# Kernel tuning notes

Hardware: AMD Instinct MI355X
Metric: run time of the kernel (lower is better)

The kernel has to match this reference:

```python
import jax, jax.numpy as jnp
import numpy as np

SUB_NO = 64
SYN_BASIS_NO = 3
T_HIST = 200
T_DATA = 100000


def setup_inputs() -> dict:
    key = jax.random.key(0)
    ks = jax.random.split(key, 5)
    # strictly-lower-triangular adjacency: each subunit integrates from ancestors
    C_den = jnp.tril((jax.random.uniform(ks[0], (SUB_NO, SUB_NO)) < 0.15).astype(jnp.float32), k=-1)
    S_conv = jax.random.normal(ks[1], (T_DATA, SUB_NO), dtype=jnp.float32)
    Y_ancest = 0.1 * jax.random.normal(ks[2], (T_DATA, SUB_NO), dtype=jnp.float32)
    # sparse binary spike trains
    Z_ancest = (jax.random.uniform(ks[3], (T_DATA, SUB_NO)) < 0.05).astype(jnp.float32)
    V_o = jnp.full((1,), -69.0, dtype=jnp.float32)
    W_sub = jnp.full((SUB_NO,), 0.25, dtype=jnp.float32)
    theta_syn = jnp.zeros((SUB_NO,), dtype=jnp.float32)
    K_spike = jnp.full((SUB_NO, SYN_BASIS_NO), 0.01, dtype=jnp.float32)
    tau_spike = jnp.arange(1.6, 1.6 + SYN_BASIS_NO, dtype=jnp.float32)
    delta_spike = jnp.zeros((SUB_NO,), dtype=jnp.float32)
    return {"S_conv": S_conv, "Y_ancest": Y_ancest, "Z_ancest": Z_ancest,
            "C_den": C_den, "V_o": V_o, "W_sub": W_sub, "theta_syn": theta_syn,
            "K_spike": K_spike, "tau_spike": tau_spike, "delta_spike": delta_spike,
            "T_hist": T_HIST}


def _ancest_kernel(K_spike, tau_spike, delta_spike, T_hist):
    # t[s, k] = max(k - delta_s, 0); kern[s, k] = sum_b (t/tau_b) exp(-t/tau_b) K[s,b]
    t = jnp.arange(T_hist, dtype=jnp.float32)[None, :] - delta_spike[:, None]
    t = jnp.maximum(t, 0.0)                                  # [sub, T_hist]
    tau = jnp.exp(tau_spike)                                 # [basis]
    t_tau = t[:, None, :] / tau[None, :, None]               # [sub, basis, T_hist]
    kern = jnp.sum(t_tau * jnp.exp(-t_tau) * K_spike[:, :, None], axis=1)
    return kern                                              # [sub, T_hist]


def reference(S_conv, Y_ancest, Z_ancest, C_den, V_o, W_sub, theta_syn,
              K_spike, tau_spike, delta_spike, T_hist):
    T_data, sub_no = S_conv.shape
    kern = _ancest_kernel(K_spike, tau_spike, delta_spike, T_hist)
    kern_f = jnp.flip(kern, axis=1)                          # matches torch.flip

    # spike_ancest[t, s, k] = sum_j C_den[s,j] Z_pad[t+k, j]  ->  precontract once
    Zc = Z_ancest @ C_den.T                                  # [T, sub]
    Zc_pad = jnp.concatenate([jnp.zeros((T_hist, sub_no), Zc.dtype), Zc], axis=0)
    # depthwise VALID conv over time: filtered[t, s] = sum_k kern_f[s,k] Zc_pad[t+k, s]
    out = jax.lax.conv_general_dilated(
        Zc_pad.T[None],                                      # [1, sub, T+T_hist]
        kern_f[:, None, :],                                  # [sub, 1, T_hist]
        window_strides=(1,), padding='VALID',
        feature_group_count=sub_no,
        dimension_numbers=('NCH', 'OIH', 'NCH'))
    filtered = out[0, :, :T_data].T                          # [T, sub]

    raw = Y_ancest @ C_den.T                                 # [T, sub]
    X_in = S_conv + theta_syn + filtered + raw
    final_Y = jax.nn.sigmoid(X_in) * W_sub + V_o
    return final_Y
```

## Files before the change

### kernel.cpp

```cpp
#include <hip/hip_runtime.h>

#define SUBS  64
#define GUARD 256
#define LB    32
#define JT    8
#define LSTR  136

typedef _Float16 f16x8 __attribute__((ext_vector_type(8)));
typedef float    f32x4 __attribute__((ext_vector_type(4)));

__device__ inline f16x8 ld_frag(const float* p) {
    float4 a = *(const float4*)p;
    float4 b = *(const float4*)(p + 4);
    f16x8 f;
    f[0]=(_Float16)a.x; f[1]=(_Float16)a.y; f[2]=(_Float16)a.z; f[3]=(_Float16)a.w;
    f[4]=(_Float16)b.x; f[5]=(_Float16)b.y; f[6]=(_Float16)b.z; f[7]=(_Float16)b.w;
    return f;
}
__device__ inline uint pkh2(float a, float b) {
    union { _Float16 h[2]; uint u; } p;
    p.h[0] = (_Float16)a; p.h[1] = (_Float16)b; return p.u;
}

#define STEP3(u)                                                                 \
    _Pragma("unroll")                                                            \
    for (int b = 0; b < 3; ++b) {                                                \
        const float yn = fmaf(twr[b], y1[b], fmaf(mr2[b], y2[b], cr[b] * (u)));  \
        y2[b] = y1[b]; y1[b] = yn;                                               \
    }
#define PAIRW(wrd) {                                                             \
    union { uint u; _Float16 h[2]; } w_; w_.u = (wrd);                           \
    STEP3((float)w_.h[0]);                                                       \
    STEP3((float)w_.h[1]); }

__global__ __launch_bounds__(256, 4) void k_mm(
    const float* __restrict__ Z, const float* __restrict__ Y,
    const float* __restrict__ C,
    const float* __restrict__ K_spike, const float* __restrict__ tau_spike,
    _Float16* __restrict__ Zt, _Float16* __restrict__ Yt,
    float* __restrict__ fb, int T, int rgz, int NB)
{
    __shared__ _Float16 ztl[SUBS * LSTR];
    __shared__ _Float16 ytl[SUBS * LSTR];
    const int tid  = threadIdx.x;
    const int lane = tid & 63;
    const int wv   = tid >> 6;
    const int lr   = lane & 15;
    const int lg   = lane >> 4;
    const int t0b  = blockIdx.x * 128;

    if (blockIdx.x < 8) {
        const int tile = blockIdx.x * 4 + (tid >> 6);
        uint4 z4 = {0, 0, 0, 0};
        ((uint4*)Zt)[(size_t)tile * 64 + (tid & 63)] = z4;
        ((uint4*)Yt)[(size_t)tile * 64 + (tid & 63)] = z4;
    } else if (blockIdx.x < 18) {
        const int tile = rgz + (blockIdx.x - 8) * 4 + (tid >> 6);
        uint4 z4 = {0, 0, 0, 0};
        ((uint4*)Zt)[(size_t)tile * 64 + (tid & 63)] = z4;
        ((uint4*)Yt)[(size_t)tile * 64 + (tid & 63)] = z4;
    }
    if (blockIdx.x == 0) {
        for (int idx = tid; idx < JT * 384; idx += 256) fb[idx] = 0.f;
    }

    f16x8 bfr[4][2];
    #pragma unroll
    for (int nt = 0; nt < 4; ++nt)
        #pragma unroll
        for (int ks = 0; ks < 2; ++ks)
            bfr[nt][ks] = ld_frag(&C[(lr + 16 * nt) * 64 + ks * 32 + lg * 8]);

    #pragma unroll
    for (int g = 0; g < 2; ++g) {
        const int t0 = t0b + wv * 32 + g * 16;
        const int rowA = t0 + lr;
        const bool okA = rowA < T;
        f16x8 az[2], ay[2];
        #pragma unroll
        for (int ks = 0; ks < 2; ++ks) {
            if (okA) {
                az[ks] = ld_frag(&Z[(size_t)rowA * 64 + ks * 32 + lg * 8]);
                ay[ks] = ld_frag(&Y[(size_t)rowA * 64 + ks * 32 + lg * 8]);
            } else {
                az[ks] = (f16x8)(_Float16)0.f;
                ay[ks] = (f16x8)(_Float16)0.f;
            }
        }

        f32x4 accZ[4], accY[4];
        #pragma unroll
        for (int nt = 0; nt < 4; ++nt) { accZ[nt] = (f32x4){0,0,0,0}; accY[nt] = (f32x4){0,0,0,0}; }
        #pragma unroll
        for (int nt = 0; nt < 4; ++nt) {
            #pragma unroll
            for (int ks = 0; ks < 2; ++ks) {
                accZ[nt] = __builtin_amdgcn_mfma_f32_16x16x32_f16(az[ks], bfr[nt][ks], accZ[nt], 0, 0, 0);
                accY[nt] = __builtin_amdgcn_mfma_f32_16x16x32_f16(ay[ks], bfr[nt][ks], accY[nt], 0, 0, 0);
            }
        }

        #pragma unroll
        for (int nt = 0; nt < 4; ++nt) {
            const int sc = lr + 16 * nt;
            const int lt = wv * 32 + g * 16 + lg * 4;
            uint2 pz, py;
            pz.x = pkh2(accZ[nt][0], accZ[nt][1]);
            pz.y = pkh2(accZ[nt][2], accZ[nt][3]);
            py.x = pkh2(accY[nt][0], accY[nt][1]);
            py.y = pkh2(accY[nt][2], accY[nt][3]);
            *(uint2*)&ztl[sc * LSTR + lt] = pz;
            *(uint2*)&ytl[sc * LSTR + lt] = py;
        }
    }

    __syncthreads();

    const int gbase = (GUARD >> 3) + blockIdx.x * 16;
    #pragma unroll
    for (int it = 0; it < 4; ++it) {
        const int chunk = it * 256 + tid;
        const int row = chunk & 63;
        const int col = chunk >> 6;
        const int tb  = t0b + col * 8;
        if (tb + 7 < T) {
            ((uint4*)Zt)[(size_t)(gbase + col) * 64 + row] =
                *(const uint4*)&ztl[row * LSTR + col * 8];
            ((uint4*)Yt)[(size_t)(gbase + col) * 64 + row] =
                *(const uint4*)&ytl[row * LSTR + col * 8];
        } else {
            #pragma unroll
            for (int h = 0; h < 8; ++h)
                if (tb + h < T) {
                    Zt[(size_t)(gbase + col) * 512 + row * 8 + h] = ztl[row * LSTR + col * 8 + h];
                    Yt[(size_t)(gbase + col) * 512 + row * 8 + h] = ytl[row * LSTR + col * 8 + h];
                }
        }
    }

    const int grun = blockIdx.x * 4 + wv;
    if (grun < NB) {
        float twr[3], mr2[3], cr[3];
        #pragma unroll
        for (int b = 0; b < 3; ++b) {
            const float tau = __expf(tau_spike[b]);
            const float r   = __expf(-1.0f / tau);
            twr[b] = 2.0f * r;
            mr2[b] = -r * r;
            cr[b]  = K_spike[lane * 3 + b] / tau * r;
        }
        const uint* zr = (const uint*)ztl + lane * (LSTR / 2) + wv * 16;
        float y1[3] = {0.f, 0.f, 0.f}, y2[3] = {0.f, 0.f, 0.f};
        uint xa[8];
        #pragma unroll
        for (int k = 0; k < 8; ++k) xa[k] = zr[k];
        #pragma unroll
        for (int k = 0; k < 8; ++k) PAIRW(xa[k]);
        #pragma unroll
        for (int k = 0; k < 8; ++k) xa[k] = zr[8 + k];
        #pragma unroll
        for (int k = 0; k < 8; ++k) PAIRW(xa[k]);
        float* fout = fb + (size_t)(grun + JT) * 384;
        #pragma unroll
        for (int b = 0; b < 3; ++b) {
            fout[(2 * b)     * 64 + lane] = y1[b];
            fout[(2 * b + 1) * 64 + lane] = y2[b];
        }
    }
}

#define EMIT(o, f) {                                                             \
    const int t_ = t0 + (o);                                                     \
    if (t_ < T) {                                                                \
        union { uint u; _Float16 h[2]; } wy_; wy_.u = ywd[(o) >> 1];             \
        union { uint u; _Float16 h[2]; } wp_; wp_.u = spk[(o) >> 1];             \
        const float xin_ = (float)wy_.h[(o) & 1] + (float)wp_.h[(o) & 1] + (f);  \
        const float sig_ = 1.0f / (1.0f + __expf(-xin_));                        \
        out[(size_t)t_ * 64 + s] = fmaf(sig_, wsub, vo);                         \
    } }

__global__ __launch_bounds__(256, 3) void k_iir2(
    const _Float16* __restrict__ Zt, const _Float16* __restrict__ Yt,
    const float* __restrict__ S,
    const float* __restrict__ K_spike, const float* __restrict__ tau_spike,
    const float* __restrict__ delta_spike, const float* __restrict__ theta,
    const float* __restrict__ W, const float* __restrict__ Vo,
    const float* __restrict__ fb, float* __restrict__ out, int T, int NB)
{
    const int tid = threadIdx.x;
    const int s   = tid & 63;
    const int wv  = tid >> 6;
    const int i   = blockIdx.x * 4 + wv;
    if (i >= NB) return;
    const int t0 = i * LB;

    float twr[3], mr2[3], cr[3], taus[3];
    #pragma unroll
    for (int b = 0; b < 3; ++b) {
        const float tau = __expf(tau_spike[b]);
        taus[b] = tau;
        const float r = __expf(-1.0f / tau);
        twr[b] = 2.0f * r;
        mr2[b] = -r * r;
        cr[b]  = K_spike[s * 3 + b] / tau * r;
    }
    int dl = (int)rintf(delta_spike[s]);
    dl = min(max(dl, 0), 30);
    const float th   = theta[s];
    const float wsub = W[s];
    const float vo   = Vo[0];

    float y1[3], y2[3];

    if (__all(dl == 0)) {
        float aL[3], bL[3], cL[3], dL[3];
        #pragma unroll
        for (int b = 0; b < 3; ++b) {
            const float r   = 0.5f * twr[b];
            const float rm1 = __expf(-(float)(LB - 1) / taus[b]);
            const float rl  = rm1 * r;
            const float rp  = rl * r;
            aL[b] = (float)(LB + 1) * rl;
            bL[b] = -(float)LB * rp;
            cL[b] = (float)LB * rm1;
            dL[b] = -(float)(LB - 1) * rl;
        }
        {
            const float* fq = fb + (size_t)i * 384;
            #pragma unroll
            for (int b = 0; b < 3; ++b) {
                y1[b] = fq[(2 * b) * 64 + s];
                y2[b] = fq[(2 * b + 1) * 64 + s];
            }
        }
        #pragma unroll
        for (int j = 7; j >= 1; --j) {
            const float* fq = fb + (size_t)(i + JT - j) * 384;
            #pragma unroll
            for (int b = 0; b < 3; ++b) {
                const float f1 = fq[(2 * b) * 64 + s];
                const float f2 = fq[(2 * b + 1) * 64 + s];
                const float n1 = fmaf(aL[b], y1[b], fmaf(bL[b], y2[b], f1));
                const float n2 = fmaf(cL[b], y1[b], fmaf(dL[b], y2[b], f2));
                y1[b] = n1; y2[b] = n2;
            }
        }

        const uint4* xb = (const uint4*)Zt + (size_t)(32 + 4 * i) * 64 + s;
        const uint4 x0 = xb[0], x1 = xb[64], x2 = xb[128], x3 = xb[192];
        const uint4* yb = (const uint4*)Yt + (size_t)(32 + 4 * i) * 64 + s;
        const uint4 yv0 = yb[0], yv1 = yb[64], yv2 = yb[128], yv3 = yb[192];

        uint spk[16];
        #pragma unroll
        for (int p = 0; p < 16; ++p) {
            const int t1 = min(t0 + 2 * p,     T - 1);
            const int t2 = min(t0 + 2 * p + 1, T - 1);
            spk[p] = pkh2(S[(size_t)t1 * 64 + s] + th, S[(size_t)t2 * 64 + s] + th);
        }

        const uint xw[15] = { x0.x, x0.y, x0.z, x0.w, x1.x, x1.y, x1.z, x1.w,
                              x2.x, x2.y, x2.z, x2.w, x3.x, x3.y, x3.z };
        const uint ywd[16] = { yv0.x, yv0.y, yv0.z, yv0.w, yv1.x, yv1.y, yv1.z, yv1.w,
                               yv2.x, yv2.y, yv2.z, yv2.w, yv3.x, yv3.y, yv3.z, yv3.w };

        EMIT(0, y2[0] + y2[1] + y2[2]);
        EMIT(1, y1[0] + y1[1] + y1[2]);
        #pragma unroll
        for (int w = 0; w < 15; ++w) {
            union { uint u; _Float16 h[2]; } wx; wx.u = xw[w];
            STEP3((float)wx.h[0]);
            EMIT(2 + 2 * w, y1[0] + y1[1] + y1[2]);
            STEP3((float)wx.h[1]);
            EMIT(3 + 2 * w, y1[0] + y1[1] + y1[2]);
        }
    } else {
        y1[0] = y1[1] = y1[2] = 0.f;
        y2[0] = y2[1] = y2[2] = 0.f;
        const int xi0 = t0 - 226 - dl;
        for (int k = 0; k < 224 + LB; ++k) {
            const int h = GUARD + xi0 + k;
            const float u = (float)Zt[(size_t)(h >> 3) * 512 + s * 8 + (h & 7)];
            STEP3(u);
            const int o = k - 224;
            if (o >= 0) {
                const int t = t0 + o;
                if (t < T) {
                    const int hy = GUARD + t;
                    const float yc = (float)Yt[(size_t)(hy >> 3) * 512 + s * 8 + (hy & 7)];
                    const float xin = yc + S[(size_t)t * 64 + s] + th
                                      + y1[0] + y1[1] + y1[2];
                    const float sig = 1.0f / (1.0f + __expf(-xin));
                    out[(size_t)t * 64 + s] = fmaf(sig, wsub, vo);
                }
            }
        }
    }
}

extern "C" void kernel_launch(void* const* d_in, const int* in_sizes, int n_in,
                              void* d_out, int out_size, void* d_ws, size_t ws_size,
                              hipStream_t stream)
{
    const float* S     = (const float*)d_in[0];
    const float* Y     = (const float*)d_in[1];
    const float* Z     = (const float*)d_in[2];
    const float* C     = (const float*)d_in[3];
    const float* Vo    = (const float*)d_in[4];
    const float* W     = (const float*)d_in[5];
    const float* theta = (const float*)d_in[6];
    const float* K     = (const float*)d_in[7];
    const float* tau   = (const float*)d_in[8];
    const float* delta = (const float*)d_in[9];
    const int T  = in_sizes[0] / SUBS;
    const int NB = (T + LB - 1) / LB;

    const int rgz    = (GUARD + T + 7) >> 3;
    const int ntiles = rgz + 44;
    _Float16* Zt = (_Float16*)d_ws;
    _Float16* Yt = (_Float16*)((char*)d_ws + (size_t)ntiles * 1024);
    float*    fb = (float*)((char*)d_ws + (size_t)ntiles * 2048);

    k_mm<<<(T + 127) / 128, 256, 0, stream>>>(Z, Y, C, K, tau, Zt, Yt, fb, T, rgz, NB);
    k_iir2<<<(NB + 3) / 4, 256, 0, stream>>>(Zt, Yt, S, K, tau, delta, theta,
                                             W, Vo, fb, (float*)d_out, T, NB);
}
```

Baseline: 46.55 us.

## Fold S_conv and theta into matmul stage output, vectorize partial-state layout

The first kernel now adds S_conv and theta to the Y@C^T accumulator, so it stores a single fp16 bias tile instead of Y-projection data alone. The recurrence/emit kernel then reads one combined tile and no longer loads S. The per-block IIR partial states are stored interleaved per subunit, so each is written and read with float4/float2 accesses. Guard-tile zeroing is skipped when all delays are zero, and the tail store is vectorised. This cuts global traffic in the second kernel and raises its occupancy hint, but the S loads in the first kernel are strided, and rounding S+theta to fp16 adds precision error.

```diff
diff --git a/kernel.cpp b/kernel.cpp
--- a/kernel.cpp
+++ b/kernel.cpp
@@ -35,9 +35,11 @@
 
 __global__ __launch_bounds__(256, 4) void k_mm(
     const float* __restrict__ Z, const float* __restrict__ Y,
-    const float* __restrict__ C,
+    const float* __restrict__ S, const float* __restrict__ C,
+    const float* __restrict__ theta,
     const float* __restrict__ K_spike, const float* __restrict__ tau_spike,
-    _Float16* __restrict__ Zt, _Float16* __restrict__ Yt,
+    const float* __restrict__ delta_spike,
+    _Float16* __restrict__ Zt, _Float16* __restrict__ Bt,
     float* __restrict__ fb, int T, int rgz, int NB)
 {
     __shared__ _Float16 ztl[SUBS * LSTR];
@@ -49,19 +51,25 @@
     const int lg   = lane >> 4;
     const int t0b  = blockIdx.x * 128;
 
-    if (blockIdx.x < 8) {
-        const int tile = blockIdx.x * 4 + (tid >> 6);
-        uint4 z4 = {0, 0, 0, 0};
-        ((uint4*)Zt)[(size_t)tile * 64 + (tid & 63)] = z4;
-        ((uint4*)Yt)[(size_t)tile * 64 + (tid & 63)] = z4;
-    } else if (blockIdx.x < 18) {
-        const int tile = rgz + (blockIdx.x - 8) * 4 + (tid >> 6);
-        uint4 z4 = {0, 0, 0, 0};
-        ((uint4*)Zt)[(size_t)tile * 64 + (tid & 63)] = z4;
-        ((uint4*)Yt)[(size_t)tile * 64 + (tid & 63)] = z4;
-    }
+    int dl = (int)rintf(delta_spike[lane]);
+    dl = min(max(dl, 0), 30);
+    const bool alldl0 = __all(dl == 0);
+
     if (blockIdx.x == 0) {
-        for (int idx = tid; idx < JT * 384; idx += 256) fb[idx] = 0.f;
+        for (int idx = tid; idx < JT * 512; idx += 256) fb[idx] = 0.f;
+    }
+    if (!alldl0) {
+        if (blockIdx.x < 8) {
+            const int tile = blockIdx.x * 4 + wv;
+            uint4 z4 = {0, 0, 0, 0};
+            ((uint4*)Zt)[(size_t)tile * 64 + lane] = z4;
+            ((uint4*)Bt)[(size_t)tile * 64 + lane] = z4;
+        } else if (blockIdx.x < 18) {
+            const int tile = rgz + (blockIdx.x - 8) * 4 + wv;
+            uint4 z4 = {0, 0, 0, 0};
+            ((uint4*)Zt)[(size_t)tile * 64 + lane] = z4;
+            ((uint4*)Bt)[(size_t)tile * 64 + lane] = z4;
+        }
     }
 
     f16x8 bfr[4][2];
@@ -70,6 +78,10 @@
         #pragma unroll
         for (int ks = 0; ks < 2; ++ks)
             bfr[nt][ks] = ld_frag(&C[(lr + 16 * nt) * 64 + ks * 32 + lg * 8]);
+
+    float th4[4];
+    #pragma unroll
+    for (int nt = 0; nt < 4; ++nt) th4[nt] = theta[lr + 16 * nt];
 
     #pragma unroll
     for (int g = 0; g < 2; ++g) {
@@ -97,6 +109,16 @@
             for (int ks = 0; ks < 2; ++ks) {
                 accZ[nt] = __builtin_amdgcn_mfma_f32_16x16x32_f16(az[ks], bfr[nt][ks], accZ[nt], 0, 0, 0);
                 accY[nt] = __builtin_amdgcn_mfma_f32_16x16x32_f16(ay[ks], bfr[nt][ks], accY[nt], 0, 0, 0);
+            }
+        }
+
+        #pragma unroll
+        for (int nt = 0; nt < 4; ++nt) {
+            const int sc = lr + 16 * nt;
+            #pragma unroll
+            for (int r = 0; r < 4; ++r) {
+                const int t = t0 + lg * 4 + r;
+                if (t < T) accY[nt][r] += S[(size_t)t * 64 + sc] + th4[nt];
             }
         }
 
@@ -126,15 +148,18 @@
         if (tb + 7 < T) {
             ((uint4*)Zt)[(size_t)(gbase + col) * 64 + row] =
                 *(const uint4*)&ztl[row * LSTR + col * 8];
-            ((uint4*)Yt)[(size_t)(gbase + col) * 64 + row] =
+            ((uint4*)Bt)[(size_t)(gbase + col) * 64 + row] =
                 *(const uint4*)&ytl[row * LSTR + col * 8];
         } else {
+            union { ushort u[8]; uint4 v; } vz, vb;
             #pragma unroll
-            for (int h = 0; h < 8; ++h)
-                if (tb + h < T) {
-                    Zt[(size_t)(gbase + col) * 512 + row * 8 + h] = ztl[row * LSTR + col * 8 + h];
-                    Yt[(size_t)(gbase + col) * 512 + row * 8 + h] = ytl[row * LSTR + col * 8 + h];
-                }
+            for (int h = 0; h < 8; ++h) {
+                const bool ok = (tb + h < T);
+                vz.u[h] = ok ? ((const ushort*)ztl)[row * LSTR + col * 8 + h] : (ushort)0;
+                vb.u[h] = ok ? ((const ushort*)ytl)[row * LSTR + col * 8 + h] : (ushort)0;
+            }
+            ((uint4*)Zt)[(size_t)(gbase + col) * 64 + row] = vz.v;
+            ((uint4*)Bt)[(size_t)(gbase + col) * 64 + row] = vb.v;
         }
     }
 
@@ -151,39 +176,27 @@
         }
         const uint* zr = (const uint*)ztl + lane * (LSTR / 2) + wv * 16;
         float y1[3] = {0.f, 0.f, 0.f}, y2[3] = {0.f, 0.f, 0.f};
-        uint xa[8];
-        #pragma unroll
-        for (int k = 0; k < 8; ++k) xa[k] = zr[k];
-        #pragma unroll
-        for (int k = 0; k < 8; ++k) PAIRW(xa[k]);
-        #pragma unroll
-        for (int k = 0; k < 8; ++k) xa[k] = zr[8 + k];
-        #pragma unroll
-        for (int k = 0; k < 8; ++k) PAIRW(xa[k]);
-        float* fout = fb + (size_t)(grun + JT) * 384;
-        #pragma unroll
-        for (int b = 0; b < 3; ++b) {
-            fout[(2 * b)     * 64 + lane] = y1[b];
-            fout[(2 * b + 1) * 64 + lane] = y2[b];
-        }
+        #pragma unroll
+        for (int k = 0; k < 16; ++k) PAIRW(zr[k]);
+        float* fout = fb + (size_t)(grun + JT) * 512 + lane * 8;
+        *(float4*)fout       = make_float4(y1[0], y2[0], y1[1], y2[1]);
+        *(float2*)(fout + 4) = make_float2(y1[2], y2[2]);
     }
 }
 
 #define EMIT(o, f) {                                                             \
     const int t_ = t0 + (o);                                                     \
     if (t_ < T) {                                                                \
-        union { uint u; _Float16 h[2]; } wy_; wy_.u = ywd[(o) >> 1];             \
-        union { uint u; _Float16 h[2]; } wp_; wp_.u = spk[(o) >> 1];             \
-        const float xin_ = (float)wy_.h[(o) & 1] + (float)wp_.h[(o) & 1] + (f);  \
+        union { uint u; _Float16 h[2]; } wb_; wb_.u = bwd[(o) >> 1];             \
+        const float xin_ = (float)wb_.h[(o) & 1] + (f);                          \
         const float sig_ = 1.0f / (1.0f + __expf(-xin_));                        \
         out[(size_t)t_ * 64 + s] = fmaf(sig_, wsub, vo);                         \
     } }
 
-__global__ __launch_bounds__(256, 3) void k_iir2(
-    const _Float16* __restrict__ Zt, const _Float16* __restrict__ Yt,
-    const float* __restrict__ S,
+__global__ __launch_bounds__(256, 4) void k_iir2(
+    const _Float16* __restrict__ Zt, const _Float16* __restrict__ Bt,
     const float* __restrict__ K_spike, const float* __restrict__ tau_spike,
-    const float* __restrict__ delta_spike, const float* __restrict__ theta,
+    const float* __restrict__ delta_spike,
     const float* __restrict__ W, const float* __restrict__ Vo,
     const float* __restrict__ fb, float* __restrict__ out, int T, int NB)
 {
@@ -206,11 +219,8 @@
     }
     int dl = (int)rintf(delta_spike[s]);
     dl = min(max(dl, 0), 30);
-    const float th   = theta[s];
     const float wsub = W[s];
     const float vo   = Vo[0];
-
-    float y1[3], y2[3];
 
     if (__all(dl == 0)) {
         float aL[3], bL[3], cL[3], dL[3];
@@ -225,44 +235,38 @@
             cL[b] = (float)LB * rm1;
             dL[b] = -(float)(LB - 1) * rl;
         }
+        float y1[3], y2[3];
         {
-            const float* fq = fb + (size_t)i * 384;
+            const float* fq = fb + (size_t)i * 512 + s * 8;
+            const float4 lo = *(const float4*)fq;
+            const float2 hi = *(const float2*)(fq + 4);
+            y1[0] = lo.x; y2[0] = lo.y; y1[1] = lo.z; y2[1] = lo.w;
+            y1[2] = hi.x; y2[2] = hi.y;
+        }
+        #pragma unroll
+        for (int j = 7; j >= 1; --j) {
+            const float* fq = fb + (size_t)(i + JT - j) * 512 + s * 8;
+            const float4 lo = *(const float4*)fq;
+            const float2 hi = *(const float2*)(fq + 4);
+            const float f1[3] = { lo.x, lo.z, hi.x };
+            const float f2[3] = { lo.y, lo.w, hi.y };
             #pragma unroll
             for (int b = 0; b < 3; ++b) {
-                y1[b] = fq[(2 * b) * 64 + s];
-                y2[b] = fq[(2 * b + 1) * 64 + s];
-            }
-        }
-        #pragma unroll
-        for (int j = 7; j >= 1; --j) {
-            const float* fq = fb + (size_t)(i + JT - j) * 384;
-            #pragma unroll
-            for (int b = 0; b < 3; ++b) {
-                const float f1 = fq[(2 * b) * 64 + s];
-                const float f2 = fq[(2 * b + 1) * 64 + s];
-                const float n1 = fmaf(aL[b], y1[b], fmaf(bL[b], y2[b], f1));
-                const float n2 = fmaf(cL[b], y1[b], fmaf(dL[b], y2[b], f2));
+                const float n1 = fmaf(aL[b], y1[b], fmaf(bL[b], y2[b], f1[b]));
+                const float n2 = fmaf(cL[b], y1[b], fmaf(dL[b], y2[b], f2[b]));
                 y1[b] = n1; y2[b] = n2;
             }
         }
 
         const uint4* xb = (const uint4*)Zt + (size_t)(32 + 4 * i) * 64 + s;
         const uint4 x0 = xb[0], x1 = xb[64], x2 = xb[128], x3 = xb[192];
-        const uint4* yb = (const uint4*)Yt + (size_t)(32 + 4 * i) * 64 + s;
-        const uint4 yv0 = yb[0], yv1 = yb[64], yv2 = yb[128], yv3 = yb[192];
-
-        uint spk[16];
-        #pragma unroll
-        for (int p = 0; p < 16; ++p) {
-            const int t1 = min(t0 + 2 * p,     T - 1);
-            const int t2 = min(t0 + 2 * p + 1, T - 1);
-            spk[p] = pkh2(S[(size_t)t1 * 64 + s] + th, S[(size_t)t2 * 64 + s] + th);
-        }
-
-        const uint xw[15] = { x0.x, x0.y, x0.z, x0.w, x1.x, x1.y, x1.z, x1.w,
-                              x2.x, x2.y, x2.z, x2.w, x3.x, x3.y, x3.z };
-        const uint ywd[16] = { yv0.x, yv0.y, yv0.z, yv0.w, yv1.x, yv1.y, yv1.z, yv1.w,
-                               yv2.x, yv2.y, yv2.z, yv2.w, yv3.x, yv3.y, yv3.z, yv3.w };
+        const uint4* bb = (const uint4*)Bt + (size_t)(32 + 4 * i) * 64 + s;
+        const uint4 b0 = bb[0], b1 = bb[64], b2 = bb[128], b3 = bb[192];
+
+        const uint xw[15]  = { x0.x, x0.y, x0.z, x0.w, x1.x, x1.y, x1.z, x1.w,
+                               x2.x, x2.y, x2.z, x2.w, x3.x, x3.y, x3.z };
+        const uint bwd[16] = { b0.x, b0.y, b0.z, b0.w, b1.x, b1.y, b1.z, b1.w,
+                               b2.x, b2.y, b2.z, b2.w, b3.x, b3.y, b3.z, b3.w };
 
         EMIT(0, y2[0] + y2[1] + y2[2]);
         EMIT(1, y1[0] + y1[1] + y1[2]);
@@ -275,8 +279,7 @@
             EMIT(3 + 2 * w, y1[0] + y1[1] + y1[2]);
         }
     } else {
-        y1[0] = y1[1] = y1[2] = 0.f;
-        y2[0] = y2[1] = y2[2] = 0.f;
+        float y1[3] = {0.f, 0.f, 0.f}, y2[3] = {0.f, 0.f, 0.f};
         const int xi0 = t0 - 226 - dl;
         for (int k = 0; k < 224 + LB; ++k) {
             const int h = GUARD + xi0 + k;
@@ -287,9 +290,8 @@
                 const int t = t0 + o;
                 if (t < T) {
                     const int hy = GUARD + t;
-                    const float yc = (float)Yt[(size_t)(hy >> 3) * 512 + s * 8 + (hy & 7)];
-                    const float xin = yc + S[(size_t)t * 64 + s] + th
-                                      + y1[0] + y1[1] + y1[2];
+                    const float bv = (float)Bt[(size_t)(hy >> 3) * 512 + s * 8 + (hy & 7)];
+                    const float xin = bv + y1[0] + y1[1] + y1[2];
                     const float sig = 1.0f / (1.0f + __expf(-xin));
                     out[(size_t)t * 64 + s] = fmaf(sig, wsub, vo);
                 }
@@ -318,10 +320,11 @@
     const int rgz    = (GUARD + T + 7) >> 3;
     const int ntiles = rgz + 44;
     _Float16* Zt = (_Float16*)d_ws;
-    _Float16* Yt = (_Float16*)((char*)d_ws + (size_t)ntiles * 1024);
+    _Float16* Bt = (_Float16*)((char*)d_ws + (size_t)ntiles * 1024);
     float*    fb = (float*)((char*)d_ws + (size_t)ntiles * 2048);
 
-    k_mm<<<(T + 127) / 128, 256, 0, stream>>>(Z, Y, C, K, tau, Zt, Yt, fb, T, rgz, NB);
-    k_iir2<<<(NB + 3) / 4, 256, 0, stream>>>(Zt, Yt, S, K, tau, delta, theta,
-                                             W, Vo, fb, (float*)d_out, T, NB);
-}
+    k_mm<<<(T + 127) / 128, 256, 0, stream>>>(Z, Y, S, C, theta, K, tau, delta,
+                                              Zt, Bt, fb, T, rgz, NB);
+    k_iir2<<<(NB + 3) / 4, 256, 0, stream>>>(Zt, Bt, K, tau, delta, W, Vo, fb,
+                                             (float*)d_out, T, NB);
+}
```

After: 52.66 us. 1.13x slower.
